# Kernel optimization log

Hardware: AMD Instinct MI355X
Metric: run time of the kernel (lower is better)

Reference implementation:

```python
import jax, jax.numpy as jnp
import numpy as np

B, NX, NY, NZ, C, MAX_PTS = 4, 512, 512, 1, 64, 32
P_PER_B = 16384            # non-empty pillars per frame (unique cells)
MASK_RATIO = 0.7


def setup_inputs() -> dict:
    key = jax.random.key(0)
    kf, kn, ks, kc = jax.random.split(key, 4)
    grid = NZ * NX * NY
    # unique linear pillar locations per batch element -> deterministic scatter-set
    lin = jnp.stack([
        jax.random.permutation(jax.random.fold_in(kc, b), grid)[:P_PER_B]
        for b in range(B)
    ])  # [B, P]
    y = (lin // NX).reshape(-1)
    x = (lin % NX).reshape(-1)
    bidx = jnp.repeat(jnp.arange(B), P_PER_B)
    voxel_coords = jnp.stack(
        [bidx, jnp.zeros_like(bidx), y, x], axis=1).astype(jnp.int32)  # [M,4] = (b,z,y,x)
    M = B * P_PER_B
    pillar_features = jax.random.normal(kf, (M, C), dtype=jnp.float32)
    voxel_num_points = jax.random.randint(kn, (M,), 1, MAX_PTS + 1, dtype=jnp.int32)
    K = int(M * (1.0 - MASK_RATIO))
    select_index = jnp.sort(jax.random.permutation(ks, M)[:K]).astype(jnp.int32)
    return {
        "pillar_features": pillar_features,
        "voxel_coords": voxel_coords,
        "voxel_num_points": voxel_num_points,
        "select_index": select_index,
    }


def reference(pillar_features, voxel_coords, voxel_num_points, select_index):
    grid = NZ * NX * NY
    # per-pillar flat index into the batched dense grid:
    # within-frame index = z + y*nx + x (nz == 1), offset by batch*grid
    flat = (voxel_coords[:, 0] * grid
            + voxel_coords[:, 1]
            + voxel_coords[:, 2] * NX
            + voxel_coords[:, 3])  # [M]

    fdt = pillar_features.dtype
    occupancy = jnp.zeros(B * grid, dtype=fdt).at[flat].set(1.0).reshape(B, NY, NX)
    points_number = (jnp.zeros(B * grid, dtype=voxel_num_points.dtype)
                     .at[flat].set(voxel_num_points).reshape(B, NY, NX))
    density = (jnp.zeros(B * grid, dtype=fdt)
               .at[flat].set(voxel_num_points.astype(fdt) / MAX_PTS)
               .reshape(B, NY, NX))

    # scatter only the unmasked (selected) pillar features into the dense BEV grid
    flat_sel = flat[select_index]               # [K]
    feats_sel = pillar_features[select_index]   # [K, C]
    spatial = (jnp.zeros((B * grid, C), dtype=fdt)
               .at[flat_sel].set(feats_sel)
               .reshape(B, grid, C)
               .transpose(0, 2, 1)
               .reshape(B, C * NZ, NY, NX))
    return spatial, occupancy, density, points_number
```

## Files before the change

### kernel.cpp

```cpp
#include <hip/hip_runtime.h>

#define NXD   512
#define NYD   512
#define CD    64
#define BD    4
#define GRIDC (NXD * NYD)

#define ROW_MASK   0x1FFFF
#define NPTS_SHIFT 17
#define SEL_FLAG   (1 << 23)

typedef float f32x4 __attribute__((ext_vector_type(4)));
typedef int   i32x4 __attribute__((ext_vector_type(4)));


__global__ void build_map_kernel(const int* __restrict__ coords,
                                 const int* __restrict__ sel,
                                 const int* __restrict__ npts,
                                 int* __restrict__ map, int M, int K) {
    int i = blockIdx.x * blockDim.x + threadIdx.x;
    if (i < M) {
        int b = coords[4 * i + 0];
        int z = coords[4 * i + 1];
        int y = coords[4 * i + 2];
        int x = coords[4 * i + 3];
        int cell = b * GRIDC + z + y * NXD + x;
        atomicOr(map + cell, (i + 1) | (npts[i] << NPTS_SHIFT));
    } else if (i < M + K) {
        int r = sel[i - M];
        int b = coords[4 * r + 0];
        int z = coords[4 * r + 1];
        int y = coords[4 * r + 2];
        int x = coords[4 * r + 3];
        int cell = b * GRIDC + z + y * NXD + x;
        atomicOr(map + cell, SEL_FLAG);
    }
}

__global__ __launch_bounds__(256) void fused_fill_kernel(
        const float* __restrict__ feats,
        const int*   __restrict__ map,
        const float* __restrict__ zerobuf,
        float* __restrict__ out) {
    const size_t base = (size_t)blockIdx.x * 1024;
    const int b   = (int)(base >> 18);
    const int cif = (int)(base & (GRIDC - 1));
    const int t   = threadIdx.x;
    const size_t cbase = base + (size_t)t * 4;

    const i32x4 m4 = *reinterpret_cast<const i32x4*>(map + cbase);
    const int rows[4] = {m4.x, m4.y, m4.z, m4.w};

    const float* p[4];
    #pragma unroll
    for (int j = 0; j < 4; ++j) {
        int m = rows[j];
        p[j] = (m & SEL_FLAG) ? (feats + ((size_t)((m & ROW_MASK) - 1) << 6))
                              : zerobuf;
    }

    float* __restrict__ spatial = out;
    const size_t sp_off = (size_t)b * ((size_t)CD * GRIDC) + (size_t)(cif + t * 4);

    #pragma unroll 2
    for (int cg = 0; cg < 16; ++cg) {
        f32x4 f0 = *reinterpret_cast<const f32x4*>(p[0] + 4 * cg);
        f32x4 f1 = *reinterpret_cast<const f32x4*>(p[1] + 4 * cg);
        f32x4 f2 = *reinterpret_cast<const f32x4*>(p[2] + 4 * cg);
        f32x4 f3 = *reinterpret_cast<const f32x4*>(p[3] + 4 * cg);
        #pragma unroll
        for (int q = 0; q < 4; ++q) {
            f32x4 v;
            v[0] = f0[q]; v[1] = f1[q]; v[2] = f2[q]; v[3] = f3[q];
            __builtin_nontemporal_store(
                v, reinterpret_cast<f32x4*>(spatial + sp_off + (size_t)(4 * cg + q) * GRIDC));
        }
    }

    const size_t spatial_elems = (size_t)BD * CD * GRIDC;
    const size_t map_elems     = (size_t)BD * GRIDC;
    float* __restrict__ occ  = out + spatial_elems;
    float* __restrict__ dens = occ + map_elems;
    float* __restrict__ pnum = dens + map_elems;

    f32x4 o, d, pn;
    #pragma unroll
    for (int j = 0; j < 4; ++j) {
        int m = rows[j];
        if (m != 0) {
            float n = (float)((m >> NPTS_SHIFT) & 63);
            o[j] = 1.0f;
            d[j] = n * (1.0f / 32.0f);
            pn[j] = n;
        } else {
            o[j] = 0.f; d[j] = 0.f; pn[j] = 0.f;
        }
    }
    __builtin_nontemporal_store(o,  reinterpret_cast<f32x4*>(occ  + cbase));
    __builtin_nontemporal_store(d,  reinterpret_cast<f32x4*>(dens + cbase));
    __builtin_nontemporal_store(pn, reinterpret_cast<f32x4*>(pnum + cbase));
}


__global__ void scatter_meta_kernel(const int* __restrict__ coords,
                                    const int* __restrict__ npts,
                                    float* __restrict__ occ,
                                    float* __restrict__ dens,
                                    float* __restrict__ pnum,
                                    int M) {
    int i = blockIdx.x * blockDim.x + threadIdx.x;
    if (i >= M) return;
    int b = coords[4 * i + 0];
    int z = coords[4 * i + 1];
    int y = coords[4 * i + 2];
    int x = coords[4 * i + 3];
    int cell = b * GRIDC + z + y * NXD + x;
    float n = (float)npts[i];
    occ[cell]  = 1.0f;
    dens[cell] = n * (1.0f / 32.0f);
    pnum[cell] = n;
}

__global__ void scatter_spatial_kernel(const float* __restrict__ feats,
                                       const int* __restrict__ coords,
                                       const int* __restrict__ sel,
                                       float* __restrict__ spatial,
                                       int K) {
    int group = blockIdx.x * (blockDim.x >> 6) + (threadIdx.x >> 6);
    int c     = threadIdx.x & 63;
    if (group >= K) return;
    int row = sel[group];
    int b = coords[4 * row + 0];
    int z = coords[4 * row + 1];
    int y = coords[4 * row + 2];
    int x = coords[4 * row + 3];
    int cell = z + y * NXD + x;
    float v = feats[(size_t)row * CD + c];
    spatial[(size_t)b * ((size_t)CD * GRIDC) + (size_t)c * GRIDC + (size_t)cell] = v;
}

extern "C" void kernel_launch(void* const* d_in, const int* in_sizes, int n_in,
                              void* d_out, int out_size, void* d_ws, size_t ws_size,
                              hipStream_t stream) {
    const float* feats  = (const float*)d_in[0];
    const int*   coords = (const int*)d_in[1];
    const int*   npts   = (const int*)d_in[2];
    const int*   sel    = (const int*)d_in[3];

    const int M = in_sizes[2];
    const int K = in_sizes[3];

    float* out = (float*)d_out;
    const size_t map_bytes = (size_t)BD * GRIDC * sizeof(int);
    const size_t zero_bytes = CD * sizeof(float);

    if (ws_size >= map_bytes + zero_bytes) {
        int* map = (int*)d_ws;
        const float* zerobuf = (const float*)((char*)d_ws + map_bytes);
        (void)hipMemsetAsync(d_ws, 0, map_bytes + zero_bytes, stream);
        build_map_kernel<<<(M + K + 255) / 256, 256, 0, stream>>>(
            coords, sel, npts, map, M, K);
        fused_fill_kernel<<<(BD * GRIDC) / 1024, 256, 0, stream>>>(
            feats, map, zerobuf, out);
    } else {
        size_t spatial_elems = (size_t)BD * CD * GRIDC;
        size_t map_elems     = (size_t)BD * GRIDC;
        float* occ  = out + spatial_elems;
        float* dens = occ + map_elems;
        float* pnum = dens + map_elems;
        (void)hipMemsetAsync(d_out, 0, (size_t)out_size * sizeof(float), stream);
        scatter_meta_kernel<<<(M + 255) / 256, 256, 0, stream>>>(
            coords, npts, occ, dens, pnum, M);
        scatter_spatial_kernel<<<(K + 3) / 4, 256, 0, stream>>>(
            feats, coords, sel, out, K);
    }
}
```

Before: 66.49 us.

## Split fill kernel into one block per output chunk and channel plane

```diff
diff --git a/kernel.cpp b/kernel.cpp
--- a/kernel.cpp
+++ b/kernel.cpp
@@ -9,6 +9,10 @@
 #define ROW_MASK   0x1FFFF
 #define NPTS_SHIFT 17
 #define SEL_FLAG   (1 << 23)
+
+#define CHUNKS_PER_PLANE (GRIDC / 1024)
+#define SPATIAL_BLOCKS   (BD * CD * CHUNKS_PER_PLANE)
+#define META_BLOCKS      (BD * GRIDC / 1024)
 
 typedef float f32x4 __attribute__((ext_vector_type(4)));
 typedef int   i32x4 __attribute__((ext_vector_type(4)));
@@ -37,68 +41,65 @@
     }
 }
 
-__global__ __launch_bounds__(256) void fused_fill_kernel(
+__global__ __launch_bounds__(256) void linear_fill_kernel(
         const float* __restrict__ feats,
         const int*   __restrict__ map,
         const float* __restrict__ zerobuf,
         float* __restrict__ out) {
-    const size_t base = (size_t)blockIdx.x * 1024;
-    const int b   = (int)(base >> 18);
-    const int cif = (int)(base & (GRIDC - 1));
+    const int bid = blockIdx.x;
     const int t   = threadIdx.x;
-    const size_t cbase = base + (size_t)t * 4;
 
-    const i32x4 m4 = *reinterpret_cast<const i32x4*>(map + cbase);
-    const int rows[4] = {m4.x, m4.y, m4.z, m4.w};
+    if (bid < SPATIAL_BLOCKS) {
+        const int b     = bid >> 14;
+        const int c     = (bid >> 8) & 63;
+        const int chunk = bid & 255;
+        const int cell0 = chunk * 1024 + t * 4;
 
-    const float* p[4];
-    #pragma unroll
-    for (int j = 0; j < 4; ++j) {
-        int m = rows[j];
-        p[j] = (m & SEL_FLAG) ? (feats + ((size_t)((m & ROW_MASK) - 1) << 6))
-                              : zerobuf;
+        const i32x4 m4 = *reinterpret_cast<const i32x4*>(
+            map + (size_t)b * GRIDC + cell0);
+        const int rows[4] = {m4.x, m4.y, m4.z, m4.w};
+
+        f32x4 v;
+        #pragma unroll
+        for (int j = 0; j < 4; ++j) {
+            int m = rows[j];
+            const float* p = (m & SEL_FLAG)
+                ? (feats + ((size_t)((m & ROW_MASK) - 1) << 6))
+                : zerobuf;
+            v[j] = p[c];
+        }
+        __builtin_nontemporal_store(
+            v, reinterpret_cast<f32x4*>(out + (size_t)bid * 1024 + t * 4));
+    } else {
+        const int mid = bid - SPATIAL_BLOCKS;
+        const size_t cbase = (size_t)mid * 1024 + t * 4;
+
+        const i32x4 m4 = *reinterpret_cast<const i32x4*>(map + cbase);
+        const int rows[4] = {m4.x, m4.y, m4.z, m4.w};
+
+        const size_t spatial_elems = (size_t)BD * CD * GRIDC;
+        const size_t map_elems     = (size_t)BD * GRIDC;
+        float* __restrict__ occ  = out + spatial_elems;
+        float* __restrict__ dens = occ + map_elems;
+        float* __restrict__ pnum = dens + map_elems;
+
+        f32x4 o, d, pn;
+        #pragma unroll
+        for (int j = 0; j < 4; ++j) {
+            int m = rows[j];
+            if (m != 0) {
+                float n = (float)((m >> NPTS_SHIFT) & 63);
+                o[j] = 1.0f;
+                d[j] = n * (1.0f / 32.0f);
+                pn[j] = n;
+            } else {
+                o[j] = 0.f; d[j] = 0.f; pn[j] = 0.f;
+            }
+        }
+        __builtin_nontemporal_store(o,  reinterpret_cast<f32x4*>(occ  + cbase));
+        __builtin_nontemporal_store(d,  reinterpret_cast<f32x4*>(dens + cbase));
+        __builtin_nontemporal_store(pn, reinterpret_cast<f32x4*>(pnum + cbase));
     }
-
-    float* __restrict__ spatial = out;
-    const size_t sp_off = (size_t)b * ((size_t)CD * GRIDC) + (size_t)(cif + t * 4);
-
-    #pragma unroll 2
-    for (int cg = 0; cg < 16; ++cg) {
-        f32x4 f0 = *reinterpret_cast<const f32x4*>(p[0] + 4 * cg);
-        f32x4 f1 = *reinterpret_cast<const f32x4*>(p[1] + 4 * cg);
-        f32x4 f2 = *reinterpret_cast<const f32x4*>(p[2] + 4 * cg);
-        f32x4 f3 = *reinterpret_cast<const f32x4*>(p[3] + 4 * cg);
-        #pragma unroll
-        for (int q = 0; q < 4; ++q) {
-            f32x4 v;
-            v[0] = f0[q]; v[1] = f1[q]; v[2] = f2[q]; v[3] = f3[q];
-            __builtin_nontemporal_store(
-                v, reinterpret_cast<f32x4*>(spatial + sp_off + (size_t)(4 * cg + q) * GRIDC));
-        }
-    }
-
-    const size_t spatial_elems = (size_t)BD * CD * GRIDC;
-    const size_t map_elems     = (size_t)BD * GRIDC;
-    float* __restrict__ occ  = out + spatial_elems;
-    float* __restrict__ dens = occ + map_elems;
-    float* __restrict__ pnum = dens + map_elems;
-
-    f32x4 o, d, pn;
-    #pragma unroll
-    for (int j = 0; j < 4; ++j) {
-        int m = rows[j];
-        if (m != 0) {
-            float n = (float)((m >> NPTS_SHIFT) & 63);
-            o[j] = 1.0f;
-            d[j] = n * (1.0f / 32.0f);
-            pn[j] = n;
-        } else {
-            o[j] = 0.f; d[j] = 0.f; pn[j] = 0.f;
-        }
-    }
-    __builtin_nontemporal_store(o,  reinterpret_cast<f32x4*>(occ  + cbase));
-    __builtin_nontemporal_store(d,  reinterpret_cast<f32x4*>(dens + cbase));
-    __builtin_nontemporal_store(pn, reinterpret_cast<f32x4*>(pnum + cbase));
 }
 
 
@@ -151,7 +152,7 @@
     const int K = in_sizes[3];
 
     float* out = (float*)d_out;
-    const size_t map_bytes = (size_t)BD * GRIDC * sizeof(int);
+    const size_t map_bytes  = (size_t)BD * GRIDC * sizeof(int);
     const size_t zero_bytes = CD * sizeof(float);
 
     if (ws_size >= map_bytes + zero_bytes) {
@@ -160,7 +161,7 @@
         (void)hipMemsetAsync(d_ws, 0, map_bytes + zero_bytes, stream);
         build_map_kernel<<<(M + K + 255) / 256, 256, 0, stream>>>(
             coords, sel, npts, map, M, K);
-        fused_fill_kernel<<<(BD * GRIDC) / 1024, 256, 0, stream>>>(
+        linear_fill_kernel<<<SPATIAL_BLOCKS + META_BLOCKS, 256, 0, stream>>>(
             feats, map, zerobuf, out);
     } else {
         size_t spatial_elems = (size_t)BD * CD * GRIDC;
```

Result: faster. 57.97 us (median of 2 runs) (-12.8%).
